# Kernel optimization log

Measured on AMD Instinct MI355X. Metric: run time of the kernel, lower is better.

## Reference

```python
import jax, jax.numpy as jnp
import numpy as np
from jax import lax

GS = 29          # grid_size
DW = 15          # displacement_width
DR = 0.4         # disp_range
N = GS ** 3      # 24389 control points
P = DW ** 2      # 225 in-plane displacements
WIN = (1, 1, 3, 3, 1)
ONE = (1, 1, 1, 1, 1)


def _axis(n):
    # align_corners=False pixel-center coords in [-1, 1], as torch affine_grid
    return (2.0 * jnp.arange(n, dtype=jnp.float32) + 1.0) / n - 1.0


def make_grids():
    a = _axis(GS)
    zc, yc, xc = jnp.meshgrid(a, a, a, indexing='ij')
    grid_xyz = jnp.stack([xc, yc, zc], -1).reshape(-1, 3)  # (N,3) xyz, d-major flatten
    s = DR * _axis(DW)
    A, B = jnp.meshgrid(s, s, indexing='ij')
    Z = jnp.zeros_like(A)
    sx = jnp.stack([B, A, Z], -1).reshape(-1, 3)  # z=0 plane: (s[w], s[h], 0)
    sy = jnp.stack([B, Z, A], -1).reshape(-1, 3)  # y=0 plane: (s[w], 0, s[d])
    sz = jnp.stack([Z, B, A], -1).reshape(-1, 3)  # x=0 plane: (0, s[h], s[d])
    shift_2d = jnp.stack([sx, sy, sz], axis=1)    # (P,3,3): [disp, plane, xyz]
    return grid_xyz, shift_2d


def trilerp(vol, coords, border):
    # vol (C,D,H,W); coords (...,3) normalized xyz; align_corners=False trilinear
    C, D, H, W = vol.shape
    vflat = vol.reshape(C, -1)
    x, y, z = coords[..., 0], coords[..., 1], coords[..., 2]
    ix = 0.5 * ((x + 1.0) * W - 1.0)
    iy = 0.5 * ((y + 1.0) * H - 1.0)
    iz = 0.5 * ((z + 1.0) * D - 1.0)
    x0 = jnp.floor(ix); y0 = jnp.floor(iy); z0 = jnp.floor(iz)
    fx, fy, fz = ix - x0, iy - y0, iz - z0
    x0 = x0.astype(jnp.int32); y0 = y0.astype(jnp.int32); z0 = z0.astype(jnp.int32)
    out = 0.0
    for dz in (0, 1):
        wz = fz if dz else 1.0 - fz
        zi = z0 + dz
        for dy in (0, 1):
            wy = fy if dy else 1.0 - fy
            yi = y0 + dy
            for dx in (0, 1):
                wx = fx if dx else 1.0 - fx
                xi = x0 + dx
                w = wx * wy * wz
                xc = jnp.clip(xi, 0, W - 1)
                yc = jnp.clip(yi, 0, H - 1)
                zc = jnp.clip(zi, 0, D - 1)
                if not border:  # padding_mode='zeros'
                    inb = ((xi >= 0) & (xi < W) & (yi >= 0) & (yi < H) & (zi >= 0) & (zi < D))
                    w = w * inb.astype(vol.dtype)
                idx = (zc * H + yc) * W + xc
                out = out + vflat[:, idx] * w
    return out  # (C, *coords.shape[:-1])


def pad_dh(x):
    # ReplicationPad3d((0,0,2,2,2,2)) on a 5D tensor: pad dims 2 and 3 by 2
    return jnp.pad(x, ((0, 0), (0, 0), (2, 2), (2, 2), (0, 0)), mode='edge')


def minpool(x):
    # -MaxPool3d((3,3,1))(-x)
    return -lax.reduce_window(-x, -jnp.inf, lax.max, WIN, ONE, 'VALID')


def avgpool(x):
    # AvgPool3d((3,3,1), stride=1)
    return lax.reduce_window(x, 0.0, lax.add, WIN, ONE, 'VALID') / 9.0


def grid_smooth(cost):
    # (1,N,DW,DW,3) -> two 3x3 avg passes over the 29^3 control grid (d,h axes)
    cp = cost.transpose(2, 3, 4, 0, 1).reshape(1, 3 * P, GS, GS, GS)
    cp = avgpool(avgpool(pad_dh(cp)))
    return cp.transpose(0, 2, 3, 4, 1).reshape(1, N, DW, DW, 3)


def setup_inputs() -> dict:
    key = jax.random.key(0)
    k1, k2 = jax.random.split(key)
    C, V = 8, 64
    feat00 = jax.random.normal(k1, (1, C, V, V, V), jnp.float32)
    feat50 = jax.random.normal(k2, (1, C, V, V, V), jnp.float32)
    grid_xyz, shift_2d = make_grids()
    shift_2d_min = jnp.array(jnp.broadcast_to(shift_2d[None, None], (1, N, P, 3, 3)))
    alpha = jnp.array([1.0, 0.1, 1.0, 1.0, 0.1, 5.0], jnp.float32)
    return {"feat00": feat00, "feat50": feat50, "shift_2d_min": shift_2d_min,
            "grid_xyz": grid_xyz, "shift_2d": shift_2d, "alpha": alpha}


def reference(feat00, feat50, shift_2d_min, grid_xyz, shift_2d, alpha):
    grid29 = grid_xyz.reshape(GS, GS * GS, 3)
    sm = shift_2d_min.reshape(GS, GS * GS, P, 3, 3)
    f00, f50 = feat00[0], feat50[0]

    def chunk(args):
        g, s = args                                                # (841,3), (841,P,3,3)
        mov = trilerp(f50, g[:, None, None, :] + s, border=True)   # (C,841,P,3)
        fix = trilerp(f00, g, border=False)                        # (C,841)
        ssd = jnp.sum((fix[:, :, None, None] - mov) ** 2, axis=0)  # (841,P,3)
        return alpha[1] + alpha[0] * ssd

    pdd = lax.map(chunk, (grid29, sm)).reshape(1, N, DW, DW, 3)
    cost = avgpool(minpool(pad_dh(pdd)))
    cost = alpha[4] + alpha[2] * pdd + alpha[3] * grid_smooth(cost)
    cost = avgpool(minpool(pad_dh(cost)))
    cost_avg = grid_smooth(cost).reshape(N, P, 3)
    cost_soft = jax.nn.softmax(-alpha[5] * cost_avg, axis=1)
    pred_xyz = 0.5 * jnp.einsum('npk,pkd->nd', cost_soft, shift_2d)
    return cost_soft.reshape(N, 1, DW, DW, 3), pred_xyz, cost_avg
```

## Files before the change

kernel.cpp:

```cpp
#include <hip/hip_runtime.h>
#include <math.h>

#define GS   29
#define GS2  841
#define NCP  24389
#define DW   15
#define PP   225
#define CH   675
#define CC   8
#define VV   64
#define V3   262144

typedef __attribute__((ext_vector_type(8))) _Float16 half8;

__device__ __forceinline__ float sv(int i) {
    return 0.4f * ((2.f * i + 1.f) * (1.f / 15.f) - 1.f);
}

__global__ __launch_bounds__(256) void make_vols(const float* __restrict__ in,
                                                 _Float16* __restrict__ volA,
                                                 _Float16* __restrict__ volB) {
    int v = blockIdx.x * 256 + threadIdx.x;
    if (v >= V3) return;
    int z = v >> 12, y = (v >> 6) & 63, x = v & 63;
    half8 h;
#pragma unroll
    for (int c = 0; c < CC; c++) h[c] = (_Float16)in[c * V3 + v];
    *(half8*)(volA + (size_t)v * 8) = h;
    *(half8*)(volB + (size_t)((((z << 6) | x) << 6) | y) * 8) = h;
}

__global__ __launch_bounds__(256) void pdd_pool_n(const float* __restrict__ f00,
                                                  const _Float16* __restrict__ volA,
                                                  const _Float16* __restrict__ volB,
                                                  const float* __restrict__ grid,
                                                  const float* __restrict__ alpha,
                                                  _Float16* __restrict__ pdd,
                                                  _Float16* __restrict__ pool) {
    int n = blockIdx.x;
    int tid = threadIdx.x;
    __shared__ __align__(16) _Float16 fixh[8];
    __shared__ float rowp[CH];
    __shared__ float smin[3 * 289];

    float gx = grid[n * 3 + 0], gy = grid[n * 3 + 1], gz = grid[n * 3 + 2];

    if (tid < 8) {
        float ix = 0.5f * ((gx + 1.f) * VV - 1.f);
        float iy = 0.5f * ((gy + 1.f) * VV - 1.f);
        float iz = 0.5f * ((gz + 1.f) * VV - 1.f);
        float x0f = floorf(ix), y0f = floorf(iy), z0f = floorf(iz);
        float fx = ix - x0f, fy = iy - y0f, fz = iz - z0f;
        int x0 = (int)x0f, y0 = (int)y0f, z0 = (int)z0f;
        const float* fc = f00 + tid * V3;
        float acc = 0.f;
        for (int dz = 0; dz < 2; dz++) {
            int zi = z0 + dz; float wz = dz ? fz : 1.f - fz;
            for (int dy = 0; dy < 2; dy++) {
                int yi = y0 + dy; float wy = dy ? fy : 1.f - fy;
                for (int dx = 0; dx < 2; dx++) {
                    int xi = x0 + dx; float wx = dx ? fx : 1.f - fx;
                    if (xi >= 0 && xi < VV && yi >= 0 && yi < VV && zi >= 0 && zi < VV)
                        acc += wx * wy * wz * fc[(zi * VV + yi) * VV + xi];
                }
            }
        }
        fixh[tid] = (_Float16)acc;
    }
    __syncthreads();

    if (tid < PP) {
        int p = tid;
        int h_ = p / 15, w_ = p - 15 * h_;
        float A = sv(h_), B = sv(w_);
        half8 f8 = *(const half8*)fixh;
        float a0 = alpha[0], a1 = alpha[1];

        for (int k = 0; k < 3; k++) {
            float pu, pv, pw;
            const _Float16* vol;
            if (k == 0)      { pu = gx + B; pv = gy + A; pw = gz;     vol = volA; }
            else if (k == 1) { pu = gx + B; pv = gy;     pw = gz + A; vol = volA; }
            else             { pu = gy + B; pv = gx;     pw = gz + A; vol = volB; }

            float iu = 0.5f * ((pu + 1.f) * VV - 1.f);
            float iv = 0.5f * ((pv + 1.f) * VV - 1.f);
            float iw = 0.5f * ((pw + 1.f) * VV - 1.f);
            float u0f = floorf(iu), v0f = floorf(iv), w0f = floorf(iw);
            float fu = iu - u0f, fv = iv - v0f, fw = iw - w0f;
            int u0 = (int)u0f, v0 = (int)v0f, w0 = (int)w0f;

            int p0 = min(max(u0, 0), VV - 2);
            float wAu = (u0 < 0) ? 1.f : ((u0 >= VV - 1) ? 0.f : (1.f - fu));
            float wBu = 1.f - wAu;
            int v0c = min(max(v0, 0), VV - 1), v1c = min(max(v0 + 1, 0), VV - 1);
            int w0c = min(max(w0, 0), VV - 1), w1c = min(max(w0 + 1, 0), VV - 1);
            float wv0 = 1.f - fv, wv1 = fv;
            float ww0 = 1.f - fw, ww1 = fw;

            half8 acc = {0, 0, 0, 0, 0, 0, 0, 0};
#define PAIR(WC, VC, WGT) {                                               \
                float fA_ = (WGT) * wAu, fB_ = (WGT) * wBu;               \
                _Float16 hA_ = (_Float16)fA_, hB_ = (_Float16)fB_;        \
                half8 hA8 = {hA_, hA_, hA_, hA_, hA_, hA_, hA_, hA_};     \
                half8 hB8 = {hB_, hB_, hB_, hB_, hB_, hB_, hB_, hB_};     \
                const _Float16* vp = vol + (size_t)((((WC) * VV) + (VC)) * VV + p0) * 8; \
                half8 lo = *(const half8*)vp;                             \
                half8 hi = *(const half8*)(vp + 8);                       \
                acc += hA8 * lo;                                          \
                acc += hB8 * hi;                                          \
            }
            PAIR(w0c, v0c, ww0 * wv0)
            PAIR(w0c, v1c, ww0 * wv1)
            PAIR(w1c, v0c, ww1 * wv0)
            PAIR(w1c, v1c, ww1 * wv1)
#undef PAIR

            half8 d8 = f8 - acc;
            float ssd = 0.f;
#pragma unroll
            for (int c = 0; c < 8; c++) { float dc = (float)d8[c]; ssd = fmaf(dc, dc, ssd); }
            rowp[p * 3 + k] = a1 + a0 * ssd;
        }
    }
    __syncthreads();

    for (int idx = tid; idx < 867; idx += 256) {
        int k = idx / 289; int r = idx - 289 * k; int a = r / 17; int b = r - 17 * a;
        float mn = 1e30f;
        for (int u = 0; u < 3; u++) {
            int hh = min(max(a + u - 2, 0), 14);
            for (int v = 0; v < 3; v++) {
                int ww = min(max(b + v - 2, 0), 14);
                mn = fminf(mn, rowp[(hh * 15 + ww) * 3 + k]);
            }
        }
        smin[idx] = mn;
    }
    __syncthreads();

    for (int i = tid; i < CH; i += 256) {
        pdd[(size_t)n * CH + i] = (_Float16)rowp[i];
        int p = i / 3, k = i - 3 * p;
        int h = p / 15, w = p - 15 * h;
        float acc = 0.f;
        for (int a = 0; a < 3; a++)
            for (int b = 0; b < 3; b++)
                acc += smin[k * 289 + (h + a) * 17 + (w + b)];
        pool[(size_t)n * CH + i] = (_Float16)(acc * (1.f / 9.f));
    }
}

__global__ __launch_bounds__(256) void gs_z2_h(const _Float16* __restrict__ in,
                                               _Float16* __restrict__ out) {
    const int ZS = GS2 * CH;
    int id = blockIdx.x * 256 + threadIdx.x;
    if (id >= ZS) return;
    const float w0 = 1.f / 9.f, w1 = 2.f / 9.f, w2 = 3.f / 9.f;
    const _Float16* p = in + id;
    float v0 = (float)p[0], v1 = v0, v2 = v0;
    float v3 = (float)p[ZS], v4 = (float)p[2 * (size_t)ZS];
    for (int z = 0; z < GS; z++) {
        out[id + (size_t)z * ZS] = (_Float16)(w0 * v0 + w1 * v1 + w2 * v2 + w1 * v3 + w0 * v4);
        v0 = v1; v1 = v2; v2 = v3; v3 = v4;
        int zn = z + 3; if (zn > GS - 1) zn = GS - 1;
        v4 = (float)p[(size_t)zn * ZS];
    }
}

__global__ __launch_bounds__(256) void gs_y_cost2_h(const _Float16* __restrict__ zt,
                                                    _Float16* pc,
                                                    const float* __restrict__ alpha) {
    const int ZS = GS2 * CH, YS = GS * CH;
    int id = blockIdx.x * 256 + threadIdx.x;
    if (id >= GS * YS) return;
    int z = id / YS; int rem = id - z * YS;
    size_t base = (size_t)z * ZS + rem;
    const float w0 = 1.f / 9.f, w1 = 2.f / 9.f, w2 = 3.f / 9.f;
    float a2 = alpha[2], a3 = alpha[3], a4 = alpha[4];
    const _Float16* p = zt + base;
    float v0 = (float)p[0], v1 = v0, v2 = v0;
    float v3 = (float)p[YS], v4 = (float)p[2 * (size_t)YS];
    for (int y = 0; y < GS; y++) {
        size_t idx = base + (size_t)y * YS;
        float acc = w0 * v0 + w1 * v1 + w2 * v2 + w1 * v3 + w0 * v4;
        float cur = (float)pc[idx];
        pc[idx] = (_Float16)(a4 + a2 * cur + a3 * acc);
        v0 = v1; v1 = v2; v2 = v3; v3 = v4;
        int yn = y + 3; if (yn > GS - 1) yn = GS - 1;
        v4 = (float)p[(size_t)yn * YS];
    }
}

__global__ __launch_bounds__(256) void gs_y2_hf(const _Float16* __restrict__ zt,
                                                float* __restrict__ out) {
    const int ZS = GS2 * CH, YS = GS * CH;
    int id = blockIdx.x * 256 + threadIdx.x;
    if (id >= GS * YS) return;
    int z = id / YS; int rem = id - z * YS;
    size_t base = (size_t)z * ZS + rem;
    const float w0 = 1.f / 9.f, w1 = 2.f / 9.f, w2 = 3.f / 9.f;
    const _Float16* p = zt + base;
    float v0 = (float)p[0], v1 = v0, v2 = v0;
    float v3 = (float)p[YS], v4 = (float)p[2 * (size_t)YS];
    for (int y = 0; y < GS; y++) {
        out[base + (size_t)y * YS] = w0 * v0 + w1 * v1 + w2 * v2 + w1 * v3 + w0 * v4;
        v0 = v1; v1 = v2; v2 = v3; v3 = v4;
        int yn = y + 3; if (yn > GS - 1) yn = GS - 1;
        v4 = (float)p[(size_t)yn * YS];
    }
}

__global__ __launch_bounds__(256) void pool_h(const _Float16* __restrict__ in,
                                              _Float16* __restrict__ out) {
    int n = blockIdx.x;
    int tid = threadIdx.x;
    __shared__ float sin_[CH];
    __shared__ float smn[17 * 17 * 3];
    for (int i = tid; i < CH; i += 256) sin_[i] = (float)in[(size_t)n * CH + i];
    __syncthreads();
    for (int idx = tid; idx < 17 * 17 * 3; idx += 256) {
        int a = idx / 51; int r = idx - 51 * a; int b = r / 3; int k = r - 3 * b;
        float mn = 1e30f;
        for (int u = 0; u < 3; u++) {
            int hh = min(max(a + u - 2, 0), 14);
            for (int v = 0; v < 3; v++) {
                int ww = min(max(b + v - 2, 0), 14);
                mn = fminf(mn, sin_[(hh * 15 + ww) * 3 + k]);
            }
        }
        smn[idx] = mn;
    }
    __syncthreads();
    for (int s = tid; s < CH; s += 256) {
        int h = s / 45; int r = s - 45 * h; int w = r / 3; int k = r - 3 * w;
        float acc = 0.f;
        for (int a = 0; a < 3; a++)
            for (int b = 0; b < 3; b++)
                acc += smn[(h + a) * 51 + (w + b) * 3 + k];
        out[(size_t)n * CH + s] = (_Float16)(acc * (1.f / 9.f));
    }
}

__global__ __launch_bounds__(256) void softmax_pred2(const float* __restrict__ ca,
                                                     const float* __restrict__ alpha,
                                                     float* __restrict__ soft,
                                                     float* __restrict__ pred) {
    int n = blockIdx.x;
    int tid = threadIdx.x;
    int wave = tid >> 6, lane = tid & 63;
    __shared__ float vals[CH];
    __shared__ float partial[3][3];
    for (int i = tid; i < CH; i += 256) vals[i] = ca[(size_t)n * CH + i];
    __syncthreads();
    float a5 = alpha[5];
    if (wave < 3) {
        int k = wave;
        float v[4], e[4];
        float m = -1e30f;
#pragma unroll
        for (int j = 0; j < 4; j++) {
            int p = lane + 64 * j;
            v[j] = (p < PP) ? -a5 * vals[p * 3 + k] : -1e30f;
            m = fmaxf(m, v[j]);
        }
#pragma unroll
        for (int o = 32; o > 0; o >>= 1) m = fmaxf(m, __shfl_xor(m, o));
        float sum = 0.f;
#pragma unroll
        for (int j = 0; j < 4; j++) {
            int p = lane + 64 * j;
            e[j] = (p < PP) ? __expf(v[j] - m) : 0.f;
            sum += e[j];
        }
#pragma unroll
        for (int o = 32; o > 0; o >>= 1) sum += __shfl_xor(sum, o);
        float inv = 1.f / sum;
        float px = 0.f, py = 0.f, pz = 0.f;
#pragma unroll
        for (int j = 0; j < 4; j++) {
            int p = lane + 64 * j;
            if (p < PP) {
                float s = e[j] * inv;
                vals[p * 3 + k] = s;
                int h_ = p / 15, w_ = p - 15 * h_;
                float A = sv(h_), B = sv(w_);
                if (k == 0)      { px += s * B; py += s * A; }
                else if (k == 1) { px += s * B; pz += s * A; }
                else             { py += s * B; pz += s * A; }
            }
        }
#pragma unroll
        for (int o = 32; o > 0; o >>= 1) {
            px += __shfl_xor(px, o);
            py += __shfl_xor(py, o);
            pz += __shfl_xor(pz, o);
        }
        if (lane == 0) { partial[k][0] = px; partial[k][1] = py; partial[k][2] = pz; }
    }
    __syncthreads();
    if (tid < 3) pred[(size_t)n * 3 + tid] = 0.5f * (partial[0][tid] + partial[1][tid] + partial[2][tid]);
    for (int i = tid; i < CH; i += 256) soft[(size_t)n * CH + i] = vals[i];
}

extern "C" void kernel_launch(void* const* d_in, const int* in_sizes, int n_in,
                              void* d_out, int out_size, void* d_ws, size_t ws_size,
                              hipStream_t stream) {
    const float* f00   = (const float*)d_in[0];
    const float* f50   = (const float*)d_in[1];
    const float* grid  = (const float*)d_in[3];
    const float* alpha = (const float*)d_in[5];

    float* out0 = (float*)d_out;
    float* out1 = out0 + (size_t)NCP * CH;
    float* out2 = out1 + (size_t)NCP * 3;

    char* ws = (char*)d_ws;
    _Float16* volA = (_Float16*)ws;
    _Float16* volB = volA + (size_t)V3 * 8;
    _Float16* H0 = volB + (size_t)V3 * 8;
    _Float16* H1 = H0 + (size_t)NCP * CH;
    _Float16* H2 = H1 + (size_t)NCP * CH;

    make_vols<<<(V3 + 255) / 256, 256, 0, stream>>>(f50, volA, volB);

    pdd_pool_n<<<NCP, 256, 0, stream>>>(f00, volA, volB, grid, alpha, H0, H1);

    const int TOT = GS2 * CH;
    const int gb2 = (TOT + 255) / 256;

    gs_z2_h<<<gb2, 256, 0, stream>>>(H1, H2);
    gs_y_cost2_h<<<gb2, 256, 0, stream>>>(H2, H0, alpha);

    pool_h<<<NCP, 256, 0, stream>>>(H0, H1);
    gs_z2_h<<<gb2, 256, 0, stream>>>(H1, H2);
    gs_y2_hf<<<gb2, 256, 0, stream>>>(H2, out2);

    softmax_pred2<<<NCP, 256, 0, stream>>>(out2, alpha, out0, out1);
}
```

Baseline: 558.5 us.

## Pad rows to even width, vectorize smoothing to half2, fuse cost_avg output into softmax

Rows of the fp16 intermediate buffers are padded from 675 to 676 entries so the separable z/y smoothing kernels can load and store half2 pairs, which halves their thread count and memory transactions. The final y-smoothing now writes fp16 into a scratch buffer instead of fp32 to the output. The softmax kernel reads that fp16 data and writes the fp32 cost_avg output itself, removing one full fp32 write and read pass. The pdd sampling hoists per-axis coordinate and weight setup that the three planes share, and the pooling shared arrays use a padded planar layout. The risks are the extra precision loss from rounding cost_avg to fp16, and the padded last element of each row, which is never written but does flow through the smoothing kernels.

```diff
diff --git a/kernel.cpp b/kernel.cpp
--- a/kernel.cpp
+++ b/kernel.cpp
@@ -7,14 +7,66 @@
 #define DW   15
 #define PP   225
 #define CH   675
+#define CHP  676
 #define CC   8
 #define VV   64
 #define V3   262144
 
+#define ZS2  (GS2 * CHP / 2)
+#define YS2  (GS  * CHP / 2)
+
 typedef __attribute__((ext_vector_type(8))) _Float16 half8;
+typedef __attribute__((ext_vector_type(2))) _Float16 half2t;
 
 __device__ __forceinline__ float sv(int i) {
     return 0.4f * ((2.f * i + 1.f) * (1.f / 15.f) - 1.f);
+}
+
+__device__ __forceinline__ void axis_pair(float g, int& p0, float& wA, float& wB) {
+    float i = 0.5f * ((g + 1.f) * VV - 1.f);
+    float f0 = floorf(i);
+    float fr = i - f0;
+    int i0 = (int)f0;
+    p0 = min(max(i0, 0), VV - 2);
+    wA = (i0 < 0) ? 1.f : ((i0 >= VV - 1) ? 0.f : (1.f - fr));
+    wB = 1.f - wA;
+}
+__device__ __forceinline__ void axis_cl(float g, int& c0, int& c1, float& w0, float& w1) {
+    float i = 0.5f * ((g + 1.f) * VV - 1.f);
+    float f0 = floorf(i);
+    float fr = i - f0;
+    int i0 = (int)f0;
+    c0 = min(max(i0, 0), VV - 1);
+    c1 = min(max(i0 + 1, 0), VV - 1);
+    w0 = 1.f - fr; w1 = fr;
+}
+
+__device__ __forceinline__ float sample_ssd(const _Float16* __restrict__ vol, half8 f8,
+                                            int w0c, int w1c, float ww0, float ww1,
+                                            int v0c, int v1c, float wv0, float wv1,
+                                            int p0, float wA, float wB) {
+    half8 acc = {0, 0, 0, 0, 0, 0, 0, 0};
+#define PAIR_(WC, VC, WGT) {                                              \
+        float fA_ = (WGT) * wA, fB_ = (WGT) * wB;                         \
+        _Float16 hA_ = (_Float16)fA_, hB_ = (_Float16)fB_;                \
+        half8 hA8 = {hA_, hA_, hA_, hA_, hA_, hA_, hA_, hA_};             \
+        half8 hB8 = {hB_, hB_, hB_, hB_, hB_, hB_, hB_, hB_};             \
+        const _Float16* vp = vol + (size_t)((((WC) * VV) + (VC)) * VV + p0) * 8; \
+        half8 lo = *(const half8*)vp;                                     \
+        half8 hi = *(const half8*)(vp + 8);                               \
+        acc += hA8 * lo;                                                  \
+        acc += hB8 * hi;                                                  \
+    }
+    PAIR_(w0c, v0c, ww0 * wv0)
+    PAIR_(w0c, v1c, ww0 * wv1)
+    PAIR_(w1c, v0c, ww1 * wv0)
+    PAIR_(w1c, v1c, ww1 * wv1)
+#undef PAIR_
+    half8 d8 = f8 - acc;
+    float ssd = 0.f;
+#pragma unroll
+    for (int c = 0; c < 8; c++) { float dc = (float)d8[c]; ssd = fmaf(dc, dc, ssd); }
+    return ssd;
 }
 
 __global__ __launch_bounds__(256) void make_vols(const float* __restrict__ in,
@@ -41,7 +93,7 @@
     int tid = threadIdx.x;
     __shared__ __align__(16) _Float16 fixh[8];
     __shared__ float rowp[CH];
-    __shared__ float smin[3 * 289];
+    __shared__ float smin[3 * 306];
 
     float gx = grid[n * 3 + 0], gy = grid[n * 3 + 1], gz = grid[n * 3 + 2];
 
@@ -70,58 +122,25 @@
     __syncthreads();
 
     if (tid < PP) {
-        int p = tid;
-        int h_ = p / 15, w_ = p - 15 * h_;
+        int h_ = tid / 15, w_ = tid - 15 * h_;
         float A = sv(h_), B = sv(w_);
         half8 f8 = *(const half8*)fixh;
         float a0 = alpha[0], a1 = alpha[1];
 
-        for (int k = 0; k < 3; k++) {
-            float pu, pv, pw;
-            const _Float16* vol;
-            if (k == 0)      { pu = gx + B; pv = gy + A; pw = gz;     vol = volA; }
-            else if (k == 1) { pu = gx + B; pv = gy;     pw = gz + A; vol = volA; }
-            else             { pu = gy + B; pv = gx;     pw = gz + A; vol = volB; }
-
-            float iu = 0.5f * ((pu + 1.f) * VV - 1.f);
-            float iv = 0.5f * ((pv + 1.f) * VV - 1.f);
-            float iw = 0.5f * ((pw + 1.f) * VV - 1.f);
-            float u0f = floorf(iu), v0f = floorf(iv), w0f = floorf(iw);
-            float fu = iu - u0f, fv = iv - v0f, fw = iw - w0f;
-            int u0 = (int)u0f, v0 = (int)v0f, w0 = (int)w0f;
-
-            int p0 = min(max(u0, 0), VV - 2);
-            float wAu = (u0 < 0) ? 1.f : ((u0 >= VV - 1) ? 0.f : (1.f - fu));
-            float wBu = 1.f - wAu;
-            int v0c = min(max(v0, 0), VV - 1), v1c = min(max(v0 + 1, 0), VV - 1);
-            int w0c = min(max(w0, 0), VV - 1), w1c = min(max(w0 + 1, 0), VV - 1);
-            float wv0 = 1.f - fv, wv1 = fv;
-            float ww0 = 1.f - fw, ww1 = fw;
-
-            half8 acc = {0, 0, 0, 0, 0, 0, 0, 0};
-#define PAIR(WC, VC, WGT) {                                               \
-                float fA_ = (WGT) * wAu, fB_ = (WGT) * wBu;               \
-                _Float16 hA_ = (_Float16)fA_, hB_ = (_Float16)fB_;        \
-                half8 hA8 = {hA_, hA_, hA_, hA_, hA_, hA_, hA_, hA_};     \
-                half8 hB8 = {hB_, hB_, hB_, hB_, hB_, hB_, hB_, hB_};     \
-                const _Float16* vp = vol + (size_t)((((WC) * VV) + (VC)) * VV + p0) * 8; \
-                half8 lo = *(const half8*)vp;                             \
-                half8 hi = *(const half8*)(vp + 8);                       \
-                acc += hA8 * lo;                                          \
-                acc += hB8 * hi;                                          \
-            }
-            PAIR(w0c, v0c, ww0 * wv0)
-            PAIR(w0c, v1c, ww0 * wv1)
-            PAIR(w1c, v0c, ww1 * wv0)
-            PAIR(w1c, v1c, ww1 * wv1)
-#undef PAIR
-
-            half8 d8 = f8 - acc;
-            float ssd = 0.f;
-#pragma unroll
-            for (int c = 0; c < 8; c++) { float dc = (float)d8[c]; ssd = fmaf(dc, dc, ssd); }
-            rowp[p * 3 + k] = a1 + a0 * ssd;
-        }
+        int px0; float pxA, pxB; axis_pair(gx + B, px0, pxA, pxB);
+        int py0; float pyA, pyB; axis_pair(gy + B, py0, pyA, pyB);
+        int va0, va1; float wva0, wva1; axis_cl(gy + A, va0, va1, wva0, wva1);
+        int wa0, wa1; float wwa0, wwa1; axis_cl(gz + A, wa0, wa1, wwa0, wwa1);
+        int zb0, zb1; float wzb0, wzb1; axis_cl(gz, zb0, zb1, wzb0, wzb1);
+        int yb0, yb1; float wyb0, wyb1; axis_cl(gy, yb0, yb1, wyb0, wyb1);
+        int xb0, xb1; float wxb0, wxb1; axis_cl(gx, xb0, xb1, wxb0, wxb1);
+
+        rowp[tid * 3 + 0] = a1 + a0 * sample_ssd(volA, f8, zb0, zb1, wzb0, wzb1,
+                                                 va0, va1, wva0, wva1, px0, pxA, pxB);
+        rowp[tid * 3 + 1] = a1 + a0 * sample_ssd(volA, f8, wa0, wa1, wwa0, wwa1,
+                                                 yb0, yb1, wyb0, wyb1, px0, pxA, pxB);
+        rowp[tid * 3 + 2] = a1 + a0 * sample_ssd(volB, f8, wa0, wa1, wwa0, wwa1,
+                                                 xb0, xb1, wxb0, wxb1, py0, pyA, pyB);
     }
     __syncthreads();
 
@@ -135,79 +154,98 @@
                 mn = fminf(mn, rowp[(hh * 15 + ww) * 3 + k]);
             }
         }
-        smin[idx] = mn;
+        smin[k * 306 + a * 18 + b] = mn;
     }
     __syncthreads();
 
     for (int i = tid; i < CH; i += 256) {
-        pdd[(size_t)n * CH + i] = (_Float16)rowp[i];
+        pdd[(size_t)n * CHP + i] = (_Float16)rowp[i];
         int p = i / 3, k = i - 3 * p;
         int h = p / 15, w = p - 15 * h;
         float acc = 0.f;
         for (int a = 0; a < 3; a++)
             for (int b = 0; b < 3; b++)
-                acc += smin[k * 289 + (h + a) * 17 + (w + b)];
-        pool[(size_t)n * CH + i] = (_Float16)(acc * (1.f / 9.f));
-    }
-}
-
-__global__ __launch_bounds__(256) void gs_z2_h(const _Float16* __restrict__ in,
-                                               _Float16* __restrict__ out) {
-    const int ZS = GS2 * CH;
+                acc += smin[k * 306 + (h + a) * 18 + (w + b)];
+        pool[(size_t)n * CHP + i] = (_Float16)(acc * (1.f / 9.f));
+    }
+}
+
+__global__ __launch_bounds__(256) void gs_z2v(const half2t* __restrict__ in,
+                                              half2t* __restrict__ out) {
     int id = blockIdx.x * 256 + threadIdx.x;
-    if (id >= ZS) return;
+    if (id >= ZS2) return;
     const float w0 = 1.f / 9.f, w1 = 2.f / 9.f, w2 = 3.f / 9.f;
-    const _Float16* p = in + id;
-    float v0 = (float)p[0], v1 = v0, v2 = v0;
-    float v3 = (float)p[ZS], v4 = (float)p[2 * (size_t)ZS];
+    const half2t* p = in + id;
+    half2t h0 = p[0], h3 = p[ZS2], h4 = p[2 * (size_t)ZS2];
+    float a0 = (float)h0[0], b0 = (float)h0[1];
+    float a1 = a0, b1 = b0, a2 = a0, b2 = b0;
+    float a3 = (float)h3[0], b3 = (float)h3[1];
+    float a4 = (float)h4[0], b4 = (float)h4[1];
     for (int z = 0; z < GS; z++) {
-        out[id + (size_t)z * ZS] = (_Float16)(w0 * v0 + w1 * v1 + w2 * v2 + w1 * v3 + w0 * v4);
-        v0 = v1; v1 = v2; v2 = v3; v3 = v4;
+        half2t o;
+        o[0] = (_Float16)(w0 * a0 + w1 * a1 + w2 * a2 + w1 * a3 + w0 * a4);
+        o[1] = (_Float16)(w0 * b0 + w1 * b1 + w2 * b2 + w1 * b3 + w0 * b4);
+        out[id + (size_t)z * ZS2] = o;
+        a0 = a1; b0 = b1; a1 = a2; b1 = b2; a2 = a3; b2 = b3; a3 = a4; b3 = b4;
         int zn = z + 3; if (zn > GS - 1) zn = GS - 1;
-        v4 = (float)p[(size_t)zn * ZS];
-    }
-}
-
-__global__ __launch_bounds__(256) void gs_y_cost2_h(const _Float16* __restrict__ zt,
-                                                    _Float16* pc,
-                                                    const float* __restrict__ alpha) {
-    const int ZS = GS2 * CH, YS = GS * CH;
+        half2t hn = p[(size_t)zn * ZS2];
+        a4 = (float)hn[0]; b4 = (float)hn[1];
+    }
+}
+
+__global__ __launch_bounds__(256) void gs_y_cost2v(const half2t* __restrict__ zt,
+                                                   half2t* pc,
+                                                   const float* __restrict__ alpha) {
     int id = blockIdx.x * 256 + threadIdx.x;
-    if (id >= GS * YS) return;
-    int z = id / YS; int rem = id - z * YS;
-    size_t base = (size_t)z * ZS + rem;
+    if (id >= GS * YS2) return;
+    int z = id / YS2; int rem = id - z * YS2;
+    size_t base = (size_t)z * ZS2 + rem;
     const float w0 = 1.f / 9.f, w1 = 2.f / 9.f, w2 = 3.f / 9.f;
-    float a2 = alpha[2], a3 = alpha[3], a4 = alpha[4];
-    const _Float16* p = zt + base;
-    float v0 = (float)p[0], v1 = v0, v2 = v0;
-    float v3 = (float)p[YS], v4 = (float)p[2 * (size_t)YS];
+    float c2 = alpha[2], c3 = alpha[3], c4 = alpha[4];
+    const half2t* p = zt + base;
+    half2t h0 = p[0], h3 = p[YS2], h4 = p[2 * (size_t)YS2];
+    float a0 = (float)h0[0], b0 = (float)h0[1];
+    float a1 = a0, b1 = b0, a2 = a0, b2 = b0;
+    float a3 = (float)h3[0], b3 = (float)h3[1];
+    float a4 = (float)h4[0], b4 = (float)h4[1];
     for (int y = 0; y < GS; y++) {
-        size_t idx = base + (size_t)y * YS;
-        float acc = w0 * v0 + w1 * v1 + w2 * v2 + w1 * v3 + w0 * v4;
-        float cur = (float)pc[idx];
-        pc[idx] = (_Float16)(a4 + a2 * cur + a3 * acc);
-        v0 = v1; v1 = v2; v2 = v3; v3 = v4;
+        size_t idx = base + (size_t)y * YS2;
+        float sA = w0 * a0 + w1 * a1 + w2 * a2 + w1 * a3 + w0 * a4;
+        float sB = w0 * b0 + w1 * b1 + w2 * b2 + w1 * b3 + w0 * b4;
+        half2t cur = pc[idx];
+        half2t o;
+        o[0] = (_Float16)(c4 + c2 * (float)cur[0] + c3 * sA);
+        o[1] = (_Float16)(c4 + c2 * (float)cur[1] + c3 * sB);
+        pc[idx] = o;
+        a0 = a1; b0 = b1; a1 = a2; b1 = b2; a2 = a3; b2 = b3; a3 = a4; b3 = b4;
         int yn = y + 3; if (yn > GS - 1) yn = GS - 1;
-        v4 = (float)p[(size_t)yn * YS];
-    }
-}
-
-__global__ __launch_bounds__(256) void gs_y2_hf(const _Float16* __restrict__ zt,
-                                                float* __restrict__ out) {
-    const int ZS = GS2 * CH, YS = GS * CH;
+        half2t hn = p[(size_t)yn * YS2];
+        a4 = (float)hn[0]; b4 = (float)hn[1];
+    }
+}
+
+__global__ __launch_bounds__(256) void gs_y2v(const half2t* __restrict__ zt,
+                                              half2t* __restrict__ out) {
     int id = blockIdx.x * 256 + threadIdx.x;
-    if (id >= GS * YS) return;
-    int z = id / YS; int rem = id - z * YS;
-    size_t base = (size_t)z * ZS + rem;
+    if (id >= GS * YS2) return;
+    int z = id / YS2; int rem = id - z * YS2;
+    size_t base = (size_t)z * ZS2 + rem;
     const float w0 = 1.f / 9.f, w1 = 2.f / 9.f, w2 = 3.f / 9.f;
-    const _Float16* p = zt + base;
-    float v0 = (float)p[0], v1 = v0, v2 = v0;
-    float v3 = (float)p[YS], v4 = (float)p[2 * (size_t)YS];
+    const half2t* p = zt + base;
+    half2t h0 = p[0], h3 = p[YS2], h4 = p[2 * (size_t)YS2];
+    float a0 = (float)h0[0], b0 = (float)h0[1];
+    float a1 = a0, b1 = b0, a2 = a0, b2 = b0;
+    float a3 = (float)h3[0], b3 = (float)h3[1];
+    float a4 = (float)h4[0], b4 = (float)h4[1];
     for (int y = 0; y < GS; y++) {
-        out[base + (size_t)y * YS] = w0 * v0 + w1 * v1 + w2 * v2 + w1 * v3 + w0 * v4;
-        v0 = v1; v1 = v2; v2 = v3; v3 = v4;
+        half2t o;
+        o[0] = (_Float16)(w0 * a0 + w1 * a1 + w2 * a2 + w1 * a3 + w0 * a4);
+        o[1] = (_Float16)(w0 * b0 + w1 * b1 + w2 * b2 + w1 * b3 + w0 * b4);
+        out[base + (size_t)y * YS2] = o;
+        a0 = a1; b0 = b1; a1 = a2; b1 = b2; a2 = a3; b2 = b3; a3 = a4; b3 = b4;
         int yn = y + 3; if (yn > GS - 1) yn = GS - 1;
-        v4 = (float)p[(size_t)yn * YS];
+        half2t hn = p[(size_t)yn * YS2];
+        a4 = (float)hn[0]; b4 = (float)hn[1];
     }
 }
 
@@ -215,12 +253,17 @@
                                               _Float16* __restrict__ out) {
     int n = blockIdx.x;
     int tid = threadIdx.x;
-    __shared__ float sin_[CH];
-    __shared__ float smn[17 * 17 * 3];
-    for (int i = tid; i < CH; i += 256) sin_[i] = (float)in[(size_t)n * CH + i];
-    __syncthreads();
-    for (int idx = tid; idx < 17 * 17 * 3; idx += 256) {
-        int a = idx / 51; int r = idx - 51 * a; int b = r / 3; int k = r - 3 * b;
+    __shared__ float sin_[CHP];
+    __shared__ float smn[3 * 306];
+    const half2t* inr = (const half2t*)(in + (size_t)n * CHP);
+    for (int i2 = tid; i2 < CHP / 2; i2 += 256) {
+        half2t h = inr[i2];
+        sin_[2 * i2] = (float)h[0];
+        sin_[2 * i2 + 1] = (float)h[1];
+    }
+    __syncthreads();
+    for (int idx = tid; idx < 867; idx += 256) {
+        int k = idx / 289; int r = idx - 289 * k; int a = r / 17; int b = r - 17 * a;
         float mn = 1e30f;
         for (int u = 0; u < 3; u++) {
             int hh = min(max(a + u - 2, 0), 14);
@@ -229,29 +272,37 @@
                 mn = fminf(mn, sin_[(hh * 15 + ww) * 3 + k]);
             }
         }
-        smn[idx] = mn;
+        smn[k * 306 + a * 18 + b] = mn;
     }
     __syncthreads();
     for (int s = tid; s < CH; s += 256) {
-        int h = s / 45; int r = s - 45 * h; int w = r / 3; int k = r - 3 * w;
+        int p = s / 3, k = s - 3 * p;
+        int h = p / 15, w = p - 15 * h;
         float acc = 0.f;
         for (int a = 0; a < 3; a++)
             for (int b = 0; b < 3; b++)
-                acc += smn[(h + a) * 51 + (w + b) * 3 + k];
-        out[(size_t)n * CH + s] = (_Float16)(acc * (1.f / 9.f));
-    }
-}
-
-__global__ __launch_bounds__(256) void softmax_pred2(const float* __restrict__ ca,
+                acc += smn[k * 306 + (h + a) * 18 + (w + b)];
+        out[(size_t)n * CHP + s] = (_Float16)(acc * (1.f / 9.f));
+    }
+}
+
+__global__ __launch_bounds__(256) void softmax_pred3(const _Float16* __restrict__ ca,
                                                      const float* __restrict__ alpha,
                                                      float* __restrict__ soft,
-                                                     float* __restrict__ pred) {
+                                                     float* __restrict__ pred,
+                                                     float* __restrict__ cavg) {
     int n = blockIdx.x;
     int tid = threadIdx.x;
     int wave = tid >> 6, lane = tid & 63;
-    __shared__ float vals[CH];
+    __shared__ float vals[CHP];
+    __shared__ float sfx[CH];
     __shared__ float partial[3][3];
-    for (int i = tid; i < CH; i += 256) vals[i] = ca[(size_t)n * CH + i];
+    const half2t* inr = (const half2t*)(ca + (size_t)n * CHP);
+    for (int i2 = tid; i2 < CHP / 2; i2 += 256) {
+        half2t h = inr[i2];
+        vals[2 * i2] = (float)h[0];
+        vals[2 * i2 + 1] = (float)h[1];
+    }
     __syncthreads();
     float a5 = alpha[5];
     if (wave < 3) {
@@ -282,7 +333,7 @@
             int p = lane + 64 * j;
             if (p < PP) {
                 float s = e[j] * inv;
-                vals[p * 3 + k] = s;
+                sfx[p * 3 + k] = s;
                 int h_ = p / 15, w_ = p - 15 * h_;
                 float A = sv(h_), B = sv(w_);
                 if (k == 0)      { px += s * B; py += s * A; }
@@ -300,7 +351,10 @@
     }
     __syncthreads();
     if (tid < 3) pred[(size_t)n * 3 + tid] = 0.5f * (partial[0][tid] + partial[1][tid] + partial[2][tid]);
-    for (int i = tid; i < CH; i += 256) soft[(size_t)n * CH + i] = vals[i];
+    for (int i = tid; i < CH; i += 256) {
+        soft[(size_t)n * CH + i] = sfx[i];
+        cavg[(size_t)n * CH + i] = vals[i];
+    }
 }
 
 extern "C" void kernel_launch(void* const* d_in, const int* in_sizes, int n_in,
@@ -319,22 +373,21 @@
     _Float16* volA = (_Float16*)ws;
     _Float16* volB = volA + (size_t)V3 * 8;
     _Float16* H0 = volB + (size_t)V3 * 8;
-    _Float16* H1 = H0 + (size_t)NCP * CH;
-    _Float16* H2 = H1 + (size_t)NCP * CH;
+    _Float16* H1 = H0 + (size_t)NCP * CHP;
+    _Float16* H2 = H1 + (size_t)NCP * CHP;
 
     make_vols<<<(V3 + 255) / 256, 256, 0, stream>>>(f50, volA, volB);
 
     pdd_pool_n<<<NCP, 256, 0, stream>>>(f00, volA, volB, grid, alpha, H0, H1);
 
-    const int TOT = GS2 * CH;
-    const int gb2 = (TOT + 255) / 256;
-
-    gs_z2_h<<<gb2, 256, 0, stream>>>(H1, H2);
-    gs_y_cost2_h<<<gb2, 256, 0, stream>>>(H2, H0, alpha);
+    const int gbv = (ZS2 + 255) / 256;
+
+    gs_z2v<<<gbv, 256, 0, stream>>>((const half2t*)H1, (half2t*)H2);
+    gs_y_cost2v<<<gbv, 256, 0, stream>>>((const half2t*)H2, (half2t*)H0, alpha);
 
     pool_h<<<NCP, 256, 0, stream>>>(H0, H1);
-    gs_z2_h<<<gb2, 256, 0, stream>>>(H1, H2);
-    gs_y2_hf<<<gb2, 256, 0, stream>>>(H2, out2);
-
-    softmax_pred2<<<NCP, 256, 0, stream>>>(out2, alpha, out0, out1);
-}
+    gs_z2v<<<gbv, 256, 0, stream>>>((const half2t*)H1, (half2t*)H2);
+    gs_y2v<<<gbv, 256, 0, stream>>>((const half2t*)H2, (half2t*)H1);
+
+    softmax_pred3<<<NCP, 256, 0, stream>>>(H1, alpha, out0, out1, out2);
+}
```

Measured after the change: 573.1 us. +2.6%, slower.
